# Optimization experiments

Measured on AMD Instinct MI355X. Metric: run time of the kernel, lower is better.

## Reference

```python
import jax, jax.numpy as jnp
import numpy as np

MARGIN = 0.3
EPS = 1e-12  # matches F.normalize eps


def setup_inputs() -> dict:
    key = jax.random.key(0)
    prompts = jax.random.normal(key, (4096, 2048), dtype=jnp.float32)
    return {"prompts": prompts}


def reference(prompts):
    # L2-normalize rows (F.normalize(dim=1))
    norm = jnp.linalg.norm(prompts, axis=1, keepdims=True)
    p = prompts / jnp.maximum(norm, EPS)
    # pairwise cosine similarity [K, K]
    sim = p @ p.T
    K = sim.shape[0]
    # strict upper triangle (i < j) and strict threshold s > margin
    upper = jnp.triu(jnp.ones((K, K), dtype=bool), k=1)
    viol = upper & (sim > MARGIN)
    count = jnp.sum(viol)
    loss_sum = jnp.sum(jnp.where(viol, sim - MARGIN, jnp.zeros_like(sim)))
    # if no violating pair, loss is 0
    return jnp.where(count == 0,
                     jnp.asarray(0.0, dtype=sim.dtype),
                     loss_sum / jnp.maximum(count, 1).astype(sim.dtype))
```

## Files before the change

### kernel.cpp

```cpp
#include <hip/hip_runtime.h>
#include <hip/hip_fp8.h>
#include <stdint.h>

#define MARGIN 0.3f
#define NROWS 4096
#define DIM   2048
#define BT    128
#define BK    128
#define NB    (NROWS / BT)
#define NBLK  (NB * (NB + 1) / 2)

typedef float f32x4 __attribute__((ext_vector_type(4)));
typedef int   i32x4 __attribute__((ext_vector_type(4)));
typedef int   i32x8 __attribute__((ext_vector_type(8)));
typedef short s16x8 __attribute__((ext_vector_type(8)));

__device__ __forceinline__ unsigned char f32_to_fp8(float f) {
  __hip_fp8_e4m3 h(f);
  return (unsigned char)h.__x;
}

__device__ __forceinline__ ushort f32_to_bf16(float f) {
  uint32_t u = __float_as_uint(f);
  return (ushort)((u + 0x7FFFu + ((u >> 16) & 1u)) >> 16);
}

__device__ __forceinline__ void async_load16(const void* g, void* l) {
  __builtin_amdgcn_global_load_lds(
      (const __attribute__((address_space(1))) uint32_t*)g,
      (__attribute__((address_space(3))) uint32_t*)l, 16, 0, 0);
}

template <int FLY>
__global__ __launch_bounds__(256) void prep_kernel(const float* __restrict__ in,
                                                   unsigned char* __restrict__ pn,
                                                   float* __restrict__ invn,
                                                   float* __restrict__ accum) {
  const int row = blockIdx.x;
  const int tid = threadIdx.x;
  if (row == 0 && tid == 0) { accum[0] = 0.f; accum[1] = 0.f; }

  const float4* rp = (const float4*)(in + (size_t)row * DIM);
  float4 v0 = rp[tid * 2];
  float4 v1 = rp[tid * 2 + 1];
  float ss = v0.x*v0.x + v0.y*v0.y + v0.z*v0.z + v0.w*v0.w
           + v1.x*v1.x + v1.y*v1.y + v1.z*v1.z + v1.w*v1.w;
  #pragma unroll
  for (int off = 32; off; off >>= 1) ss += __shfl_down(ss, off);

  __shared__ float wred[4];
  __shared__ float stot;
  const int lane = tid & 63, w = tid >> 6;
  if (lane == 0) wred[w] = ss;
  __syncthreads();
  if (tid == 0) stot = wred[0] + wred[1] + wred[2] + wred[3];
  __syncthreads();
  const float inv = 1.0f / fmaxf(sqrtf(stot), 1e-12f);

  if (FLY) {
    if (tid == 0) invn[row] = inv;
  } else {
    union { unsigned char b[8]; uint2 u; } pack;
    pack.b[0] = f32_to_fp8(v0.x * inv); pack.b[1] = f32_to_fp8(v0.y * inv);
    pack.b[2] = f32_to_fp8(v0.z * inv); pack.b[3] = f32_to_fp8(v0.w * inv);
    pack.b[4] = f32_to_fp8(v1.x * inv); pack.b[5] = f32_to_fp8(v1.y * inv);
    pack.b[6] = f32_to_fp8(v1.z * inv); pack.b[7] = f32_to_fp8(v1.w * inv);
    *(uint2*)(pn + (size_t)row * DIM + tid * 8) = pack.u;
  }
}

__global__ __launch_bounds__(256) void tri_gemm(const unsigned char* __restrict__ pn,
                                                float* __restrict__ accum) {
  const int b = blockIdx.x;
  int t = (b & 7) * (NBLK / 8) + (b >> 3);
  int bi = 0;
  while (t >= NB - bi) { t -= NB - bi; ++bi; }
  const int bj = bi + t;

  __shared__ __align__(16) unsigned char Asm[BT * BK];
  __shared__ __align__(16) unsigned char Bsm[BT * BK];

  const int tid  = threadIdx.x;
  const int lane = tid & 63;
  const int w    = tid >> 6;
  const int wr   = w >> 1;
  const int wc   = w & 1;

  f32x4 acc[4][4] = {};
  const int rowA = bi * BT, rowB = bj * BT;

  const int srow  = (lane >> 3);
  const int gslot = (lane & 7) ^ srow;

  for (int k0 = 0; k0 < DIM; k0 += BK) {
    if (k0) __syncthreads();
    #pragma unroll
    for (int q = 0; q < 4; ++q) {
      const int r = w * 32 + q * 8;
      async_load16(pn + (size_t)(rowA + r + srow) * DIM + k0 + gslot * 16, Asm + r * BK);
      async_load16(pn + (size_t)(rowB + r + srow) * DIM + k0 + gslot * 16, Bsm + r * BK);
    }
    __syncthreads();

    const int fr = lane & 15, g = lane >> 4;
    i32x8 af[4], bfv[4];
    #pragma unroll
    for (int m = 0; m < 4; ++m) {
      const int ra = wr * 64 + m * 16 + fr;
      const unsigned char* base = Asm + ra * BK;
      i32x4 lo = *(const i32x4*)(base + ((2 * g)     ^ (ra & 7)) * 16);
      i32x4 hi = *(const i32x4*)(base + ((2 * g + 1) ^ (ra & 7)) * 16);
      af[m] = __builtin_shufflevector(lo, hi, 0, 1, 2, 3, 4, 5, 6, 7);
    }
    #pragma unroll
    for (int n = 0; n < 4; ++n) {
      const int rb = wc * 64 + n * 16 + fr;
      const unsigned char* base = Bsm + rb * BK;
      i32x4 lo = *(const i32x4*)(base + ((2 * g)     ^ (rb & 7)) * 16);
      i32x4 hi = *(const i32x4*)(base + ((2 * g + 1) ^ (rb & 7)) * 16);
      bfv[n] = __builtin_shufflevector(lo, hi, 0, 1, 2, 3, 4, 5, 6, 7);
    }

    #pragma unroll
    for (int m = 0; m < 4; ++m)
      #pragma unroll
      for (int n = 0; n < 4; ++n)
        acc[m][n] = __builtin_amdgcn_mfma_scale_f32_16x16x128_f8f6f4(
            af[m], bfv[n], acc[m][n],
            0, 0,
            0, 0x7F7F7F7F,
            0, 0x7F7F7F7F);
  }

  float lsum = 0.f, lcnt = 0.f;
  const int gib = rowA + wr * 64;
  const int gjb = rowB + wc * 64;
  #pragma unroll
  for (int m = 0; m < 4; ++m) {
    #pragma unroll
    for (int n = 0; n < 4; ++n) {
      #pragma unroll
      for (int r = 0; r < 4; ++r) {
        int gi = gib + m * 16 + (lane >> 4) * 4 + r;
        int gj = gjb + n * 16 + (lane & 15);
        float s = acc[m][n][r];
        if (gi < gj && s > MARGIN) { lsum += s - MARGIN; lcnt += 1.f; }
      }
    }
  }
  #pragma unroll
  for (int off = 32; off; off >>= 1) {
    lsum += __shfl_down(lsum, off);
    lcnt += __shfl_down(lcnt, off);
  }
  __shared__ float rs[4], rc[4];
  if (lane == 0) { rs[w] = lsum; rc[w] = lcnt; }
  __syncthreads();
  if (tid == 0) {
    atomicAdd(&accum[0], rs[0] + rs[1] + rs[2] + rs[3]);
    atomicAdd(&accum[1], rc[0] + rc[1] + rc[2] + rc[3]);
  }
}

__global__ __launch_bounds__(256) void tri_gemm_fly(const float* __restrict__ inF,
                                                    const float* __restrict__ invn,
                                                    float* __restrict__ accum) {
  enum { FBK = 64 };
  int t = blockIdx.x, bi = 0;
  while (t >= NB - bi) { t -= NB - bi; ++bi; }
  const int bj = bi + t;

  __shared__ __align__(16) ushort Asm[BT * FBK];
  __shared__ __align__(16) ushort Bsm[BT * FBK];

  const int tid  = threadIdx.x;
  const int lane = tid & 63;
  const int w    = tid >> 6;
  const int wr   = w >> 1, wc = w & 1;

  f32x4 acc[4][4] = {};
  const int rowA = bi * BT, rowB = bj * BT;

  for (int k0 = 0; k0 < DIM; k0 += FBK) {
    if (k0) __syncthreads();
    #pragma unroll
    for (int p = 0; p < 8; ++p) {
      int c   = p * 256 + tid;
      int isB = c >> 10;
      int cc  = c & 1023;
      int r   = cc >> 3;
      int s   = cc & 7;
      const int grow = (isB ? rowB : rowA) + r;
      const float4* src = (const float4*)(inF + (size_t)grow * DIM + k0 + s * 8);
      float4 v0 = src[0], v1 = src[1];
      int4 pack;
      ushort* h = (ushort*)&pack;
      h[0] = f32_to_bf16(v0.x); h[1] = f32_to_bf16(v0.y);
      h[2] = f32_to_bf16(v0.z); h[3] = f32_to_bf16(v0.w);
      h[4] = f32_to_bf16(v1.x); h[5] = f32_to_bf16(v1.y);
      h[6] = f32_to_bf16(v1.z); h[7] = f32_to_bf16(v1.w);
      *(int4*)((isB ? Bsm : Asm) + r * FBK + (s ^ (r & 7)) * 8) = pack;
    }
    __syncthreads();

    s16x8 af[2][4], bfv[2][4];
    const int fr = lane & 15, hi = lane >> 4;
    #pragma unroll
    for (int kk = 0; kk < 2; ++kk)
      #pragma unroll
      for (int m = 0; m < 4; ++m) {
        const int ra = wr * 64 + m * 16 + fr;
        af[kk][m] = *(const s16x8*)(Asm + ra * FBK + ((kk * 4 + hi) ^ (ra & 7)) * 8);
        const int rb = wc * 64 + m * 16 + fr;
        bfv[kk][m] = *(const s16x8*)(Bsm + rb * FBK + ((kk * 4 + hi) ^ (rb & 7)) * 8);
      }
    #pragma unroll
    for (int kk = 0; kk < 2; ++kk)
      #pragma unroll
      for (int m = 0; m < 4; ++m)
        #pragma unroll
        for (int n = 0; n < 4; ++n)
          acc[m][n] = __builtin_amdgcn_mfma_f32_16x16x32_bf16(af[kk][m], bfv[kk][n],
                                                              acc[m][n], 0, 0, 0);
  }

  float lsum = 0.f, lcnt = 0.f;
  const int gib = rowA + wr * 64;
  const int gjb = rowB + wc * 64;
  #pragma unroll
  for (int m = 0; m < 4; ++m)
    #pragma unroll
    for (int n = 0; n < 4; ++n)
      #pragma unroll
      for (int r = 0; r < 4; ++r) {
        int gi = gib + m * 16 + (lane >> 4) * 4 + r;
        int gj = gjb + n * 16 + (lane & 15);
        float s = acc[m][n][r] * invn[gi] * invn[gj];
        if (gi < gj && s > MARGIN) { lsum += s - MARGIN; lcnt += 1.f; }
      }
  #pragma unroll
  for (int off = 32; off; off >>= 1) {
    lsum += __shfl_down(lsum, off);
    lcnt += __shfl_down(lcnt, off);
  }
  __shared__ float rs[4], rc[4];
  if (lane == 0) { rs[w] = lsum; rc[w] = lcnt; }
  __syncthreads();
  if (tid == 0) {
    atomicAdd(&accum[0], rs[0] + rs[1] + rs[2] + rs[3]);
    atomicAdd(&accum[1], rc[0] + rc[1] + rc[2] + rc[3]);
  }
}

__global__ void finalize_kernel(const float* __restrict__ accum, float* __restrict__ out) {
  if (threadIdx.x == 0) out[0] = (accum[1] < 0.5f) ? 0.0f : accum[0] / accum[1];
}

extern "C" void kernel_launch(void* const* d_in, const int* in_sizes, int n_in,
                              void* d_out, int out_size, void* d_ws, size_t ws_size,
                              hipStream_t stream) {
  const float* in = (const float*)d_in[0];
  float* out = (float*)d_out;
  const size_t pn_bytes = (size_t)NROWS * DIM;

  if (ws_size >= pn_bytes + 2 * sizeof(float)) {
    unsigned char* pn = (unsigned char*)d_ws;
    float* accum = (float*)((char*)d_ws + pn_bytes);
    prep_kernel<0><<<NROWS, 256, 0, stream>>>(in, pn, nullptr, accum);
    tri_gemm<<<NBLK, 256, 0, stream>>>(pn, accum);
    finalize_kernel<<<1, 64, 0, stream>>>(accum, out);
  } else {
    float* invn  = (float*)d_ws;
    float* accum = (float*)((char*)d_ws + NROWS * sizeof(float));
    prep_kernel<1><<<NROWS, 256, 0, stream>>>(in, nullptr, invn, accum);
    tri_gemm_fly<<<NBLK, 256, 0, stream>>>(in, invn, accum);
    finalize_kernel<<<1, 64, 0, stream>>>(accum, out);
  }
}
```

Baseline: 46.69 us.

## Double-buffer LDS tiles to prefetch next K-slice during MFMA compute

Allocates two LDS buffers per operand and issues async global-to-LDS loads for the next K tile before computing the current one, swapping buffers after a single barrier per iteration. This overlaps global memory latency with matrix-core work and removes one barrier per step. It doubles LDS usage per block, which may reduce blocks resident per CU.

```diff
diff --git a/kernel.cpp b/kernel.cpp
--- a/kernel.cpp
+++ b/kernel.cpp
@@ -7,6 +7,7 @@
 #define DIM   2048
 #define BT    128
 #define BK    128
+#define NK    (DIM / BK)
 #define NB    (NROWS / BT)
 #define NBLK  (NB * (NB + 1) / 2)
 
@@ -77,8 +78,8 @@
   while (t >= NB - bi) { t -= NB - bi; ++bi; }
   const int bj = bi + t;
 
-  __shared__ __align__(16) unsigned char Asm[BT * BK];
-  __shared__ __align__(16) unsigned char Bsm[BT * BK];
+  __shared__ __align__(16) unsigned char Asm[2][BT * BK];
+  __shared__ __align__(16) unsigned char Bsm[2][BT * BK];
 
   const int tid  = threadIdx.x;
   const int lane = tid & 63;
@@ -92,22 +93,39 @@
   const int srow  = (lane >> 3);
   const int gslot = (lane & 7) ^ srow;
 
-  for (int k0 = 0; k0 < DIM; k0 += BK) {
-    if (k0) __syncthreads();
-    #pragma unroll
-    for (int q = 0; q < 4; ++q) {
-      const int r = w * 32 + q * 8;
-      async_load16(pn + (size_t)(rowA + r + srow) * DIM + k0 + gslot * 16, Asm + r * BK);
-      async_load16(pn + (size_t)(rowB + r + srow) * DIM + k0 + gslot * 16, Bsm + r * BK);
-    }
-    __syncthreads();
-
-    const int fr = lane & 15, g = lane >> 4;
+  const unsigned char* gA = pn + (size_t)(rowA + srow) * DIM + gslot * 16;
+  const unsigned char* gB = pn + (size_t)(rowB + srow) * DIM + gslot * 16;
+
+  unsigned char* Acur = Asm[0];  unsigned char* Bcur = Bsm[0];
+  unsigned char* Anx  = Asm[1];  unsigned char* Bnx  = Bsm[1];
+
+  #pragma unroll
+  for (int q = 0; q < 4; ++q) {
+    const int r = w * 32 + q * 8;
+    async_load16(gA + (size_t)r * DIM, Acur + r * BK);
+    async_load16(gB + (size_t)r * DIM, Bcur + r * BK);
+  }
+  __syncthreads();
+
+  const int fr = lane & 15, g = lane >> 4;
+
+  #pragma unroll 1
+  for (int ks = 0; ks < NK; ++ks) {
+    if (ks + 1 < NK) {
+      const int k0 = (ks + 1) * BK;
+      #pragma unroll
+      for (int q = 0; q < 4; ++q) {
+        const int r = w * 32 + q * 8;
+        async_load16(gA + (size_t)r * DIM + k0, Anx + r * BK);
+        async_load16(gB + (size_t)r * DIM + k0, Bnx + r * BK);
+      }
+    }
+
     i32x8 af[4], bfv[4];
     #pragma unroll
     for (int m = 0; m < 4; ++m) {
       const int ra = wr * 64 + m * 16 + fr;
-      const unsigned char* base = Asm + ra * BK;
+      const unsigned char* base = Acur + ra * BK;
       i32x4 lo = *(const i32x4*)(base + ((2 * g)     ^ (ra & 7)) * 16);
       i32x4 hi = *(const i32x4*)(base + ((2 * g + 1) ^ (ra & 7)) * 16);
       af[m] = __builtin_shufflevector(lo, hi, 0, 1, 2, 3, 4, 5, 6, 7);
@@ -115,7 +133,7 @@
     #pragma unroll
     for (int n = 0; n < 4; ++n) {
       const int rb = wc * 64 + n * 16 + fr;
-      const unsigned char* base = Bsm + rb * BK;
+      const unsigned char* base = Bcur + rb * BK;
       i32x4 lo = *(const i32x4*)(base + ((2 * g)     ^ (rb & 7)) * 16);
       i32x4 hi = *(const i32x4*)(base + ((2 * g + 1) ^ (rb & 7)) * 16);
       bfv[n] = __builtin_shufflevector(lo, hi, 0, 1, 2, 3, 4, 5, 6, 7);
@@ -130,6 +148,12 @@
             0, 0,
             0, 0x7F7F7F7F,
             0, 0x7F7F7F7F);
+
+    __syncthreads();
+
+    unsigned char* tp;
+    tp = Acur; Acur = Anx; Anx = tp;
+    tp = Bcur; Bcur = Bnx; Bnx = tp;
   }
 
   float lsum = 0.f, lcnt = 0.f;
```

New measurement: 54.98 us. 1.18x slower.

## Use 64x128 tiles with 2-wave blocks for finer triangular GEMM scheduling

Applied to the files above, without the earlier changes.

The FP8 triangular GEMM moves from 128x128 tiles with 4 waves to 64x128 tiles with 2 waves. The launch grows from 528 to 1056 blocks, and the block-index mapping is rewritten for the new triangular layout. The smaller tiles are meant to waste less work on diagonal tiles and to spread blocks more evenly across the many CUs. In exchange, each block reuses less data (A:B is 64:128), so more global/L2 traffic is needed per FLOP.

```diff
diff --git a/kernel.cpp b/kernel.cpp
--- a/kernel.cpp
+++ b/kernel.cpp
@@ -5,8 +5,13 @@
 #define MARGIN 0.3f
 #define NROWS 4096
 #define DIM   2048
+#define BK    128
+#define NK    (DIM / BK)
+#define BM    64
+#define BN    128
+#define NBJ   (NROWS / BN)
+#define NBLK2 1056
 #define BT    128
-#define BK    128
 #define NB    (NROWS / BT)
 #define NBLK  (NB * (NB + 1) / 2)
 
@@ -69,44 +74,50 @@
   }
 }
 
-__global__ __launch_bounds__(256) void tri_gemm(const unsigned char* __restrict__ pn,
+__global__ __launch_bounds__(128) void tri_gemm(const unsigned char* __restrict__ pn,
                                                 float* __restrict__ accum) {
   const int b = blockIdx.x;
-  int t = (b & 7) * (NBLK / 8) + (b >> 3);
-  int bi = 0;
-  while (t >= NB - bi) { t -= NB - bi; ++bi; }
-  const int bj = bi + t;
-
-  __shared__ __align__(16) unsigned char Asm[BT * BK];
-  __shared__ __align__(16) unsigned char Bsm[BT * BK];
+  int t = (b & 7) * (NBLK2 / 8) + (b >> 3);
+  int bj = 0;
+  while (t >= 2 * bj + 2) { t -= 2 * bj + 2; ++bj; }
+  const int bi = t;
+
+  __shared__ __align__(16) unsigned char Asm[BM * BK];
+  __shared__ __align__(16) unsigned char Bsm[BN * BK];
 
   const int tid  = threadIdx.x;
   const int lane = tid & 63;
   const int w    = tid >> 6;
-  const int wr   = w >> 1;
-  const int wc   = w & 1;
 
   f32x4 acc[4][4] = {};
-  const int rowA = bi * BT, rowB = bj * BT;
+  const int rowA = bi * BM, rowB = bj * BN;
 
   const int srow  = (lane >> 3);
   const int gslot = (lane & 7) ^ srow;
 
+  const unsigned char* gA = pn + (size_t)(rowA + srow) * DIM + gslot * 16;
+  const unsigned char* gB = pn + (size_t)(rowB + srow) * DIM + gslot * 16;
+
+  const int fr = lane & 15, g = lane >> 4;
+
   for (int k0 = 0; k0 < DIM; k0 += BK) {
     if (k0) __syncthreads();
     #pragma unroll
-    for (int q = 0; q < 4; ++q) {
-      const int r = w * 32 + q * 8;
-      async_load16(pn + (size_t)(rowA + r + srow) * DIM + k0 + gslot * 16, Asm + r * BK);
-      async_load16(pn + (size_t)(rowB + r + srow) * DIM + k0 + gslot * 16, Bsm + r * BK);
+    for (int q = 0; q < 12; ++q) {
+      const int c = q * 2 + w;
+      if (c < 8) {
+        async_load16(gA + (size_t)(8 * c) * DIM + k0, Asm + (8 * c) * BK);
+      } else {
+        const int r = 8 * (c - 8);
+        async_load16(gB + (size_t)r * DIM + k0, Bsm + r * BK);
+      }
     }
     __syncthreads();
 
-    const int fr = lane & 15, g = lane >> 4;
     i32x8 af[4], bfv[4];
     #pragma unroll
     for (int m = 0; m < 4; ++m) {
-      const int ra = wr * 64 + m * 16 + fr;
+      const int ra = m * 16 + fr;
       const unsigned char* base = Asm + ra * BK;
       i32x4 lo = *(const i32x4*)(base + ((2 * g)     ^ (ra & 7)) * 16);
       i32x4 hi = *(const i32x4*)(base + ((2 * g + 1) ^ (ra & 7)) * 16);
@@ -114,7 +125,7 @@
     }
     #pragma unroll
     for (int n = 0; n < 4; ++n) {
-      const int rb = wc * 64 + n * 16 + fr;
+      const int rb = w * 64 + n * 16 + fr;
       const unsigned char* base = Bsm + rb * BK;
       i32x4 lo = *(const i32x4*)(base + ((2 * g)     ^ (rb & 7)) * 16);
       i32x4 hi = *(const i32x4*)(base + ((2 * g + 1) ^ (rb & 7)) * 16);
@@ -133,8 +144,8 @@
   }
 
   float lsum = 0.f, lcnt = 0.f;
-  const int gib = rowA + wr * 64;
-  const int gjb = rowB + wc * 64;
+  const int gib = rowA;
+  const int gjb = rowB + w * 64;
   #pragma unroll
   for (int m = 0; m < 4; ++m) {
     #pragma unroll
@@ -153,12 +164,12 @@
     lsum += __shfl_down(lsum, off);
     lcnt += __shfl_down(lcnt, off);
   }
-  __shared__ float rs[4], rc[4];
+  __shared__ float rs[2], rc[2];
   if (lane == 0) { rs[w] = lsum; rc[w] = lcnt; }
   __syncthreads();
   if (tid == 0) {
-    atomicAdd(&accum[0], rs[0] + rs[1] + rs[2] + rs[3]);
-    atomicAdd(&accum[1], rc[0] + rc[1] + rc[2] + rc[3]);
+    atomicAdd(&accum[0], rs[0] + rs[1]);
+    atomicAdd(&accum[1], rc[0] + rc[1]);
   }
 }
 
@@ -267,7 +278,7 @@
     unsigned char* pn = (unsigned char*)d_ws;
     float* accum = (float*)((char*)d_ws + pn_bytes);
     prep_kernel<0><<<NROWS, 256, 0, stream>>>(in, pn, nullptr, accum);
-    tri_gemm<<<NBLK, 256, 0, stream>>>(pn, accum);
+    tri_gemm<<<NBLK2, 128, 0, stream>>>(pn, accum);
     finalize_kernel<<<1, 64, 0, stream>>>(accum, out);
   } else {
     float* invn  = (float*)d_ws;
```

Result: slower. 62.95 us (+34.8%).

## Quantize normalized rows to FP4 e2m1 and use FP4 scaled MFMA

Applied to the files above, without the earlier changes.

The prep kernel now packs each normalized row into 4-bit e2m1 values with a fixed 64x pre-scale, instead of 8-bit e4m3. The triangular GEMM loads half as many bytes per K step. It runs the scaled MFMA in FP4 mode with block scales compensating for the 64x factor, using the higher FP4 matrix throughput and less memory traffic. FP4 is very coarse, so the similarity values near the margin may carry much larger quantization error, which risks the accuracy of the loss.

```diff
diff --git a/kernel.cpp b/kernel.cpp
--- a/kernel.cpp
+++ b/kernel.cpp
@@ -1,12 +1,12 @@
 #include <hip/hip_runtime.h>
-#include <hip/hip_fp8.h>
 #include <stdint.h>
 
 #define MARGIN 0.3f
 #define NROWS 4096
 #define DIM   2048
+#define ROWB  1024
 #define BT    128
-#define BK    128
+#define NKS   16
 #define NB    (NROWS / BT)
 #define NBLK  (NB * (NB + 1) / 2)
 
@@ -15,14 +15,24 @@
 typedef int   i32x8 __attribute__((ext_vector_type(8)));
 typedef short s16x8 __attribute__((ext_vector_type(8)));
 
-__device__ __forceinline__ unsigned char f32_to_fp8(float f) {
-  __hip_fp8_e4m3 h(f);
-  return (unsigned char)h.__x;
-}
-
 __device__ __forceinline__ ushort f32_to_bf16(float f) {
   uint32_t u = __float_as_uint(f);
   return (ushort)((u + 0x7FFFu + ((u >> 16) & 1u)) >> 16);
+}
+
+__device__ __forceinline__ unsigned f32_to_fp4(float y) {
+  unsigned s = (__float_as_uint(y) >> 31) << 3;
+  float a = fabsf(y);
+  unsigned c;
+  if      (a < 0.25f) c = 0;
+  else if (a < 0.75f) c = 1;
+  else if (a < 1.25f) c = 2;
+  else if (a < 1.75f) c = 3;
+  else if (a < 2.5f)  c = 4;
+  else if (a < 3.5f)  c = 5;
+  else if (a < 5.0f)  c = 6;
+  else                c = 7;
+  return s | c;
 }
 
 __device__ __forceinline__ void async_load16(const void* g, void* l) {
@@ -60,12 +70,16 @@
   if (FLY) {
     if (tid == 0) invn[row] = inv;
   } else {
-    union { unsigned char b[8]; uint2 u; } pack;
-    pack.b[0] = f32_to_fp8(v0.x * inv); pack.b[1] = f32_to_fp8(v0.y * inv);
-    pack.b[2] = f32_to_fp8(v0.z * inv); pack.b[3] = f32_to_fp8(v0.w * inv);
-    pack.b[4] = f32_to_fp8(v1.x * inv); pack.b[5] = f32_to_fp8(v1.y * inv);
-    pack.b[6] = f32_to_fp8(v1.z * inv); pack.b[7] = f32_to_fp8(v1.w * inv);
-    *(uint2*)(pn + (size_t)row * DIM + tid * 8) = pack.u;
+    const float sc = inv * 64.0f;
+    float e[8] = {v0.x, v0.y, v0.z, v0.w, v1.x, v1.y, v1.z, v1.w};
+    uint32_t u = 0;
+    #pragma unroll
+    for (int j = 0; j < 4; ++j) {
+      unsigned lo = f32_to_fp4(e[2*j]   * sc);
+      unsigned hi = f32_to_fp4(e[2*j+1] * sc);
+      u |= (lo | (hi << 4)) << (8 * j);
+    }
+    *(uint32_t*)(pn + (size_t)row * ROWB + tid * 4) = u;
   }
 }
 
@@ -77,8 +91,8 @@
   while (t >= NB - bi) { t -= NB - bi; ++bi; }
   const int bj = bi + t;
 
-  __shared__ __align__(16) unsigned char Asm[BT * BK];
-  __shared__ __align__(16) unsigned char Bsm[BT * BK];
+  __shared__ __align__(16) unsigned char Asm[64 * 128];
+  __shared__ __align__(16) unsigned char Bsm[64 * 128];
 
   const int tid  = threadIdx.x;
   const int lane = tid & 63;
@@ -89,36 +103,37 @@
   f32x4 acc[4][4] = {};
   const int rowA = bi * BT, rowB = bj * BT;
 
-  const int srow  = (lane >> 3);
-  const int gslot = (lane & 7) ^ srow;
-
-  for (int k0 = 0; k0 < DIM; k0 += BK) {
-    if (k0) __syncthreads();
-    #pragma unroll
-    for (int q = 0; q < 4; ++q) {
-      const int r = w * 32 + q * 8;
-      async_load16(pn + (size_t)(rowA + r + srow) * DIM + k0 + gslot * 16, Asm + r * BK);
-      async_load16(pn + (size_t)(rowB + r + srow) * DIM + k0 + gslot * 16, Bsm + r * BK);
+  const int srow2 = 2 * (lane >> 3) + ((lane >> 2) & 1);
+  const int kslot = (lane & 3) ^ ((lane >> 3) & 3);
+
+  const unsigned char* gA = pn + (size_t)(rowA + srow2) * ROWB + kslot * 16;
+  const unsigned char* gB = pn + (size_t)(rowB + srow2) * ROWB + kslot * 16;
+
+  const int fr = lane & 15, g = lane >> 4;
+
+  for (int ks = 0; ks < NKS; ++ks) {
+    const int kb = ks * 64;
+    if (ks) __syncthreads();
+    #pragma unroll
+    for (int h = 0; h < 2; ++h) {
+      const int c = w + h * 4;
+      async_load16(gA + (size_t)c * (16 * ROWB) + kb, Asm + c * 1024);
+      async_load16(gB + (size_t)c * (16 * ROWB) + kb, Bsm + c * 1024);
     }
     __syncthreads();
 
-    const int fr = lane & 15, g = lane >> 4;
-    i32x8 af[4], bfv[4];
+    const i32x4 z4 = {0, 0, 0, 0};
+    i32x8 af[4], bf[4];
     #pragma unroll
     for (int m = 0; m < 4; ++m) {
       const int ra = wr * 64 + m * 16 + fr;
-      const unsigned char* base = Asm + ra * BK;
-      i32x4 lo = *(const i32x4*)(base + ((2 * g)     ^ (ra & 7)) * 16);
-      i32x4 hi = *(const i32x4*)(base + ((2 * g + 1) ^ (ra & 7)) * 16);
-      af[m] = __builtin_shufflevector(lo, hi, 0, 1, 2, 3, 4, 5, 6, 7);
-    }
-    #pragma unroll
-    for (int n = 0; n < 4; ++n) {
-      const int rb = wc * 64 + n * 16 + fr;
-      const unsigned char* base = Bsm + rb * BK;
-      i32x4 lo = *(const i32x4*)(base + ((2 * g)     ^ (rb & 7)) * 16);
-      i32x4 hi = *(const i32x4*)(base + ((2 * g + 1) ^ (rb & 7)) * 16);
-      bfv[n] = __builtin_shufflevector(lo, hi, 0, 1, 2, 3, 4, 5, 6, 7);
+      i32x4 va = *(const i32x4*)(Asm + (ra >> 1) * 128 + (ra & 1) * 64 +
+                                 ((g ^ ((ra >> 1) & 3)) * 16));
+      af[m] = __builtin_shufflevector(va, z4, 0, 1, 2, 3, 4, 5, 6, 7);
+      const int rb = wc * 64 + m * 16 + fr;
+      i32x4 vb = *(const i32x4*)(Bsm + (rb >> 1) * 128 + (rb & 1) * 64 +
+                                 ((g ^ ((rb >> 1) & 3)) * 16));
+      bf[m] = __builtin_shufflevector(vb, z4, 0, 1, 2, 3, 4, 5, 6, 7);
     }
 
     #pragma unroll
@@ -126,10 +141,10 @@
       #pragma unroll
       for (int n = 0; n < 4; ++n)
         acc[m][n] = __builtin_amdgcn_mfma_scale_f32_16x16x128_f8f6f4(
-            af[m], bfv[n], acc[m][n],
-            0, 0,
-            0, 0x7F7F7F7F,
-            0, 0x7F7F7F7F);
+            af[m], bf[n], acc[m][n],
+            4, 4,
+            0, 0x79797979,
+            0, 0x79797979);
   }
 
   float lsum = 0.f, lcnt = 0.f;
@@ -261,7 +276,7 @@
                               hipStream_t stream) {
   const float* in = (const float*)d_in[0];
   float* out = (float*)d_out;
-  const size_t pn_bytes = (size_t)NROWS * DIM;
+  const size_t pn_bytes = (size_t)NROWS * ROWB;
 
   if (ws_size >= pn_bytes + 2 * sizeof(float)) {
     unsigned char* pn = (unsigned char*)d_ws;
```

New measurement: 41.32 us. -11.5%, faster.
